# Optimization experiments

Measured on AMD Instinct MI355X. Metric: run time of the kernel, lower is better.

The kernel has to match this reference:

```python
import jax, jax.numpy as jnp
import numpy as np

B, S, Hd = 4, 2048, 1024
NH, D = 16, 64

def setup_inputs() -> dict:
    key = jax.random.key(0)
    ks = jax.random.split(key, 8)
    scale = 0.02
    return {
        "hidden_states": jax.random.normal(ks[0], (B, S, Hd), dtype=jnp.float32),
        "attention_mask": jnp.zeros((B, 1, 1, S), dtype=jnp.float32),
        "relations": jax.random.normal(ks[1], (1, 1, S, D), dtype=jnp.float32),
        "Wq": jax.random.normal(ks[2], (Hd, Hd), dtype=jnp.float32) * scale,
        "bq": jnp.zeros((Hd,), dtype=jnp.float32),
        "Wk": jax.random.normal(ks[3], (Hd, Hd), dtype=jnp.float32) * scale,
        "bk": jnp.zeros((Hd,), dtype=jnp.float32),
        "Wv": jax.random.normal(ks[4], (Hd, Hd), dtype=jnp.float32) * scale,
        "bv": jnp.zeros((Hd,), dtype=jnp.float32),
    }

def _heads(x):  # [B,S,Hd] -> [B,NH,S,D]
    return x.reshape(x.shape[0], x.shape[1], NH, D).transpose(0, 2, 1, 3)

def _rotate_half_interleaved(x):
    # stack([-x_odd, x_even], -1).reshape_as(x)
    return jnp.stack([-x[..., 1::2], x[..., ::2]], axis=-1).reshape(x.shape)

def reference(hidden_states, attention_mask, relations, Wq, bq, Wk, bk, Wv, bv):
    q = _heads(hidden_states @ Wq.T + bq)
    k = _heads(hidden_states @ Wk.T + bk)
    v = _heads(hidden_states @ Wv.T + bv)

    # interleaved rotary: cos from odd slots, sin from even slots, each repeated x2
    cos_pos = jnp.repeat(relations[..., 1::2], 2, axis=-1)  # [1,1,S,D]
    sin_pos = jnp.repeat(relations[..., ::2], 2, axis=-1)
    q = q * cos_pos + _rotate_half_interleaved(q) * sin_pos
    k = k * cos_pos + _rotate_half_interleaved(k) * sin_pos

    scores = jnp.einsum("bhqd,bhkd->bhqk", q, k) / jnp.sqrt(jnp.float32(D))
    scores = scores + attention_mask
    probs = jax.nn.softmax(scores, axis=-1)
    ctx = jnp.einsum("bhqk,bhkd->bhqd", probs, v)
    return ctx.transpose(0, 2, 1, 3).reshape(hidden_states.shape[0], hidden_states.shape[1], NH * D)
```

## Files before the change

### kernel.cpp

```cpp
#include <hip/hip_runtime.h>

typedef __attribute__((ext_vector_type(8))) short short8;
typedef __attribute__((ext_vector_type(4))) float f32x4;
typedef __attribute__((ext_vector_type(4))) unsigned int u32x4;
typedef __attribute__((ext_vector_type(2))) unsigned int u32x2;
typedef __attribute__((ext_vector_type(4))) unsigned short u16x4;
typedef __attribute__((ext_vector_type(2))) float f32x2;

#define NHEADS 16
#define DHEAD 64
#define SEQ 2048
#define BATCH 4
#define HD 1024
#define MTOT 8192

static __device__ __forceinline__ unsigned short f2b(float x) {
  unsigned u = __builtin_bit_cast(unsigned, x);
  u += 0x7fffu + ((u >> 16) & 1u);
  return (unsigned short)(u >> 16);
}

static __device__ __forceinline__ unsigned pk2(float lo, float hi) {
  unsigned a = __builtin_bit_cast(unsigned, lo);
  unsigned b = __builtin_bit_cast(unsigned, hi);
  a += 0x7fffu + ((a >> 16) & 1u);
  b += 0x7fffu + ((b >> 16) & 1u);
  return (a >> 16) | (b & 0xffff0000u);
}

static __device__ __forceinline__ void gll16(const void* g, void* l) {
  __builtin_amdgcn_global_load_lds(
      (const __attribute__((address_space(1))) unsigned int*)g,
      (__attribute__((address_space(3))) unsigned int*)l, 16, 0, 0);
}

__global__ void cvt_bf16(const float* __restrict__ src,
                         unsigned short* __restrict__ dst, int n4) {
  int i = blockIdx.x * blockDim.x + threadIdx.x;
  if (i < n4) {
    f32x4 v = ((const f32x4*)src)[i];
    u16x4 o;
    o[0] = f2b(v[0]); o[1] = f2b(v[1]); o[2] = f2b(v[2]); o[3] = f2b(v[3]);
    ((u16x4*)dst)[i] = o;
  }
}

__global__ __launch_bounds__(256) void qkv_gemm(
    const unsigned short* __restrict__ X,
    const unsigned short* __restrict__ Wall,
    const float* __restrict__ bq, const float* __restrict__ bk,
    const float* __restrict__ bv,
    const float* __restrict__ rel,
    unsigned short* __restrict__ Qo,
    unsigned short* __restrict__ Ko,
    unsigned short* __restrict__ Vt) {
  __shared__ __align__(16) unsigned short As[128 * 32];
  __shared__ __align__(16) unsigned short Bs[128 * 32];

  const int t = threadIdx.x;
  const int lane = t & 63;
  const int w = t >> 6;

  const int n = blockIdx.x;
  const int xcd = n & 7;
  const int li = n >> 3;
  const int pp = xcd * 3 + (li >> 6);
  const int bx = li & 63;
  const int by = pp & 7;
  const int bz = pp >> 3;

  const unsigned short* W = Wall + (size_t)bz * HD * HD;
  const int m0 = bx * 128;
  const int n0 = by * 128;

  f32x4 acc[4][4];
  for (int i = 0; i < 4; i++)
    for (int j = 0; j < 4; j++) acc[i][j] = (f32x4){0.f, 0.f, 0.f, 0.f};

  const int wm = (w & 1) * 64;
  const int wn = (w >> 1) * 64;
  const int cl = lane & 15;
  const int qd = lane >> 4;

  const int srow = lane >> 2;
  const int scol = (lane & 3) * 8;

  for (int k0 = 0; k0 < HD; k0 += 32) {
    __syncthreads();
#pragma unroll
    for (int j = 0; j < 2; j++) {
      int r0 = j * 64 + w * 16;
      gll16(X + (size_t)(m0 + r0 + srow) * HD + k0 + scol, As + r0 * 32);
      gll16(W + (size_t)(n0 + r0 + srow) * HD + k0 + scol, Bs + r0 * 32);
    }
    __syncthreads();

    const int fk = qd * 8;
    short8 af[4], bf[4];
#pragma unroll
    for (int i = 0; i < 4; i++)
      af[i] = *(const short8*)(As + (wm + i * 16 + cl) * 32 + fk);
#pragma unroll
    for (int j = 0; j < 4; j++)
      bf[j] = *(const short8*)(Bs + (wn + j * 16 + cl) * 32 + fk);
#pragma unroll
    for (int i = 0; i < 4; i++)
#pragma unroll
      for (int j = 0; j < 4; j++)
        acc[i][j] = __builtin_amdgcn_mfma_f32_16x16x32_bf16(af[i], bf[j],
                                                            acc[i][j], 0, 0, 0);
  }

  if (bz == 2) {
#pragma unroll
    for (int i = 0; i < 4; i++) {
#pragma unroll
      for (int j = 0; j < 4; j++) {
        int nn = n0 + wn + j * 16 + cl;
        int hh = nn >> 6, dd = nn & 63;
        int m = m0 + wm + i * 16 + qd * 4;
        int bb = m >> 11, ss = m & (SEQ - 1);
        float bn = bv[nn];
        u16x4 pk;
#pragma unroll
        for (int r = 0; r < 4; r++) pk[r] = f2b(acc[i][j][r] + bn);
        *(u16x4*)(Vt + ((size_t)((bb * NHEADS + hh) * DHEAD + dd)) * SEQ + ss) = pk;
      }
    }
  } else {
    const float* bias = (bz == 0) ? bq : bk;
    unsigned short* Out = (bz == 0) ? Qo : Ko;
#pragma unroll
    for (int i = 0; i < 4; i++) {
#pragma unroll
      for (int j = 0; j < 4; j++) {
        int nn = n0 + wn + j * 16 + cl;
        int hh = nn >> 6, dd = nn & 63;
        float bn = bias[nn];
#pragma unroll
        for (int r = 0; r < 4; r++) {
          int m = m0 + wm + i * 16 + qd * 4 + r;
          int bb = m >> 11, ss = m & (SEQ - 1);
          float x = acc[i][j][r] + bn;
          float p = __shfl_xor(x, 1);
          f32x2 sc = *(const f32x2*)(rel + ss * DHEAD + (dd & ~1));
          float y = (dd & 1) ? (x * sc[1] + p * sc[0])
                             : (x * sc[1] - p * sc[0]);
          Out[(((size_t)(bb * NHEADS + hh)) * SEQ + ss) * DHEAD + dd] = f2b(y);
        }
      }
    }
  }
}

__global__ __launch_bounds__(256, 2) void attn(
    const unsigned short* __restrict__ Q,
    const unsigned short* __restrict__ K,
    const unsigned short* __restrict__ Vt,
    const float* __restrict__ mask,
    float* __restrict__ out) {
  __shared__ __align__(16) unsigned short Ks[2][128 * 64];
  __shared__ __align__(16) unsigned short Vs[2][64 * 128];

  const int t = threadIdx.x;
  const int lane = t & 63;
  const int w = t >> 6;

  const int n = blockIdx.x;
  const int xcd = n & 7;
  const int li = n >> 3;
  const int bh = xcd * 8 + (li >> 4);
  const int qt = li & 15;

  const int b = bh >> 4, h = bh & 15;
  const int s0 = qt * 128;
  const unsigned short* Qp = Q + (size_t)bh * SEQ * DHEAD;
  const unsigned short* Kp = K + (size_t)bh * SEQ * DHEAD;
  const unsigned short* Vp = Vt + (size_t)bh * DHEAD * SEQ;

  const int cl = lane & 15;
  const int qd = lane >> 4;

  short8 qf[2][2];
#pragma unroll
  for (int mt = 0; mt < 2; mt++)
#pragma unroll
    for (int ks = 0; ks < 2; ks++)
      qf[mt][ks] = *(const short8*)(Qp + (size_t)(s0 + w * 32 + mt * 16 + cl) * DHEAD +
                                    ks * 32 + qd * 8);

  short8 onef;
#pragma unroll
  for (int j = 0; j < 8; j++) onef[j] = (short)0x3F80;

  f32x4 ov[2][4];
  f32x4 ovl[2];
#pragma unroll
  for (int mt = 0; mt < 2; mt++) {
    ovl[mt] = (f32x4){0.f, 0.f, 0.f, 0.f};
#pragma unroll
    for (int dt = 0; dt < 4; dt++) ov[mt][dt] = (f32x4){0.f, 0.f, 0.f, 0.f};
  }

  const float SCL = 0.125f * 1.4426950408889634f;
  const float MLG = 1.4426950408889634f;

  auto stage = [&](int bi, int kt) {
#pragma unroll
    for (int j = 0; j < 4; j++) {
      int r0 = w * 32 + j * 8;
      int r = r0 + (lane >> 3);
      int c = (lane & 7) ^ (r & 7);
      gll16(Kp + (size_t)(kt + r) * DHEAD + c * 8, &Ks[bi][r0 * 64]);
    }
#pragma unroll
    for (int j = 0; j < 4; j++) {
      int r0 = w * 16 + j * 4;
      int r = r0 + (lane >> 4);
      int c = (lane & 15) ^ (r & 7);
      gll16(Vp + (size_t)r * SEQ + kt + c * 8, &Vs[bi][r0 * 128]);
    }
  };

  stage(0, 0);

  for (int it = 0; it < SEQ / 128; it++) {
    const int kt = it * 128;
    const int bi = it & 1;
    __syncthreads();
    if (it + 1 < SEQ / 128) stage(1 - bi, kt + 128);
    const unsigned short* Ksb = &Ks[bi][0];
    const unsigned short* Vsb = &Vs[bi][0];

    f32x4 sc[2][8];
#pragma unroll
    for (int mt = 0; mt < 2; mt++)
#pragma unroll
      for (int nt = 0; nt < 8; nt++) sc[mt][nt] = (f32x4){0.f, 0.f, 0.f, 0.f};
#pragma unroll
    for (int ks = 0; ks < 2; ks++) {
#pragma unroll
      for (int nt = 0; nt < 8; nt++) {
        int krow = nt * 16 + cl;
        short8 kf = *(const short8*)(Ksb + krow * 64 +
                                     (((ks * 4 + qd) ^ (krow & 7)) << 3));
        sc[0][nt] = __builtin_amdgcn_mfma_f32_16x16x32_bf16(kf, qf[0][ks], sc[0][nt], 0, 0, 0);
        sc[1][nt] = __builtin_amdgcn_mfma_f32_16x16x32_bf16(kf, qf[1][ks], sc[1][nt], 0, 0, 0);
      }
    }

    f32x4 mkv[8];
#pragma unroll
    for (int nt = 0; nt < 8; nt++) {
      f32x4 mk = *(const f32x4*)(mask + b * SEQ + kt + nt * 16 + qd * 4);
      mkv[nt][0] = mk[0] * MLG; mkv[nt][1] = mk[1] * MLG;
      mkv[nt][2] = mk[2] * MLG; mkv[nt][3] = mk[3] * MLG;
    }
    unsigned pw[2][8][2];
#pragma unroll
    for (int mt = 0; mt < 2; mt++) {
#pragma unroll
      for (int nt = 0; nt < 8; nt++) {
        float p0 = __builtin_amdgcn_exp2f(sc[mt][nt][0] * SCL + mkv[nt][0]);
        float p1 = __builtin_amdgcn_exp2f(sc[mt][nt][1] * SCL + mkv[nt][1]);
        float p2 = __builtin_amdgcn_exp2f(sc[mt][nt][2] * SCL + mkv[nt][2]);
        float p3 = __builtin_amdgcn_exp2f(sc[mt][nt][3] * SCL + mkv[nt][3]);
        pw[mt][nt][0] = pk2(p0, p1);
        pw[mt][nt][1] = pk2(p2, p3);
      }
    }

#pragma unroll
    for (int c = 0; c < 4; c++) {
      u32x4 bb0 = {pw[0][2 * c][0], pw[0][2 * c][1], pw[0][2 * c + 1][0], pw[0][2 * c + 1][1]};
      u32x4 bb1 = {pw[1][2 * c][0], pw[1][2 * c][1], pw[1][2 * c + 1][0], pw[1][2 * c + 1][1]};
      short8 bf0 = __builtin_bit_cast(short8, bb0);
      short8 bf1 = __builtin_bit_cast(short8, bb1);
      ovl[0] = __builtin_amdgcn_mfma_f32_16x16x32_bf16(onef, bf0, ovl[0], 0, 0, 0);
      ovl[1] = __builtin_amdgcn_mfma_f32_16x16x32_bf16(onef, bf1, ovl[1], 0, 0, 0);
#pragma unroll
      for (int dt = 0; dt < 4; dt++) {
        int vrow = dt * 16 + cl;
        int sw = vrow & 7;
        const unsigned short* vb = Vsb + vrow * 128 + ((qd & 1) << 2);
        u32x2 v0 = *(const u32x2*)(vb + (((4 * c + (qd >> 1)) ^ sw) << 3));
        u32x2 v1 = *(const u32x2*)(vb + (((4 * c + 2 + (qd >> 1)) ^ sw) << 3));
        u32x4 vv = {v0[0], v0[1], v1[0], v1[1]};
        short8 vf = __builtin_bit_cast(short8, vv);
        ov[0][dt] = __builtin_amdgcn_mfma_f32_16x16x32_bf16(vf, bf0, ov[0][dt], 0, 0, 0);
        ov[1][dt] = __builtin_amdgcn_mfma_f32_16x16x32_bf16(vf, bf1, ov[1][dt], 0, 0, 0);
      }
    }
  }

#pragma unroll
  for (int mt = 0; mt < 2; mt++) {
    float rl = 1.0f / ovl[mt][0];
    int s = s0 + w * 32 + mt * 16 + cl;
    float* ob = out + ((size_t)b * SEQ + s) * HD + h * DHEAD;
#pragma unroll
    for (int dt = 0; dt < 4; dt++) {
      f32x4 o;
      o[0] = ov[mt][dt][0] * rl;
      o[1] = ov[mt][dt][1] * rl;
      o[2] = ov[mt][dt][2] * rl;
      o[3] = ov[mt][dt][3] * rl;
      *(f32x4*)(ob + dt * 16 + qd * 4) = o;
    }
  }
}

extern "C" void kernel_launch(void* const* d_in, const int* in_sizes, int n_in,
                              void* d_out, int out_size, void* d_ws, size_t ws_size,
                              hipStream_t stream) {
  const float* hidden = (const float*)d_in[0];
  const float* mask   = (const float*)d_in[1];
  const float* rel    = (const float*)d_in[2];
  const float* Wq     = (const float*)d_in[3];
  const float* bq     = (const float*)d_in[4];
  const float* Wk     = (const float*)d_in[5];
  const float* bk     = (const float*)d_in[6];
  const float* Wv     = (const float*)d_in[7];
  const float* bv     = (const float*)d_in[8];
  float* out = (float*)d_out;

  unsigned short* Xb = (unsigned short*)d_ws;
  unsigned short* Wb = Xb + (size_t)MTOT * HD;
  unsigned short* Qb = Wb + (size_t)3 * HD * HD;
  unsigned short* Kb = Qb + (size_t)MTOT * HD;
  unsigned short* Vb = Kb + (size_t)MTOT * HD;

  {
    int n4 = MTOT * HD / 4;
    cvt_bf16<<<n4 / 256, 256, 0, stream>>>(hidden, Xb, n4);
  }
  {
    int n4 = HD * HD / 4;
    cvt_bf16<<<n4 / 256, 256, 0, stream>>>(Wq, Wb, n4);
    cvt_bf16<<<n4 / 256, 256, 0, stream>>>(Wk, Wb + (size_t)HD * HD, n4);
    cvt_bf16<<<n4 / 256, 256, 0, stream>>>(Wv, Wb + (size_t)2 * HD * HD, n4);
  }
  qkv_gemm<<<dim3(1536), 256, 0, stream>>>(Xb, Wb, bq, bk, bv, rel, Qb, Kb, Vb);
  attn<<<dim3(1024), 256, 0, stream>>>(Qb, Kb, Vb, mask, out);
}
```

Before: 310.0 us.

## Fold softmax scale and mask into QKV epilogue, simplify attention inner loop

The 1/sqrt(D)*log2e factor moves into Q and exp(mask) into V, so the attention loop computes exp2 of raw scores with no per-element scale or mask add. The row sum is taken with an MFMA against a bf16 exp(mask) vector. The Q/K GEMM swaps MFMA operands so the epilogue can do vectorised rotary and packed stores. V is stored in a permuted column order so each V fragment is one 16-byte LDS read. The rounding-to-nearest-even bf16 pack becomes a cheaper round-half-up, and there is no max subtraction, so very negative masks or large scores may lose precision.

```diff
diff --git a/kernel.cpp b/kernel.cpp
--- a/kernel.cpp
+++ b/kernel.cpp
@@ -5,7 +5,6 @@
 typedef __attribute__((ext_vector_type(4))) unsigned int u32x4;
 typedef __attribute__((ext_vector_type(2))) unsigned int u32x2;
 typedef __attribute__((ext_vector_type(4))) unsigned short u16x4;
-typedef __attribute__((ext_vector_type(2))) float f32x2;
 
 #define NHEADS 16
 #define DHEAD 64
@@ -20,11 +19,9 @@
   return (unsigned short)(u >> 16);
 }
 
-static __device__ __forceinline__ unsigned pk2(float lo, float hi) {
-  unsigned a = __builtin_bit_cast(unsigned, lo);
-  unsigned b = __builtin_bit_cast(unsigned, hi);
-  a += 0x7fffu + ((a >> 16) & 1u);
-  b += 0x7fffu + ((b >> 16) & 1u);
+static __device__ __forceinline__ unsigned pk2h(float lo, float hi) {
+  unsigned a = __builtin_bit_cast(unsigned, lo) + 0x8000u;
+  unsigned b = __builtin_bit_cast(unsigned, hi) + 0x8000u;
   return (a >> 16) | (b & 0xffff0000u);
 }
 
@@ -45,12 +42,19 @@
   }
 }
 
+__global__ void prep_wmask(const float* __restrict__ m,
+                           unsigned short* __restrict__ wm, int n) {
+  int i = blockIdx.x * blockDim.x + threadIdx.x;
+  if (i < n) wm[i] = f2b(__expf(m[i]));
+}
+
 __global__ __launch_bounds__(256) void qkv_gemm(
     const unsigned short* __restrict__ X,
     const unsigned short* __restrict__ Wall,
     const float* __restrict__ bq, const float* __restrict__ bk,
     const float* __restrict__ bv,
     const float* __restrict__ rel,
+    const float* __restrict__ mask,
     unsigned short* __restrict__ Qo,
     unsigned short* __restrict__ Ko,
     unsigned short* __restrict__ Vt) {
@@ -103,51 +107,72 @@
 #pragma unroll
     for (int j = 0; j < 4; j++)
       bf[j] = *(const short8*)(Bs + (wn + j * 16 + cl) * 32 + fk);
-#pragma unroll
-    for (int i = 0; i < 4; i++)
-#pragma unroll
-      for (int j = 0; j < 4; j++)
-        acc[i][j] = __builtin_amdgcn_mfma_f32_16x16x32_bf16(af[i], bf[j],
-                                                            acc[i][j], 0, 0, 0);
+    if (bz < 2) {
+#pragma unroll
+      for (int i = 0; i < 4; i++)
+#pragma unroll
+        for (int j = 0; j < 4; j++)
+          acc[i][j] = __builtin_amdgcn_mfma_f32_16x16x32_bf16(bf[j], af[i],
+                                                              acc[i][j], 0, 0, 0);
+    } else {
+#pragma unroll
+      for (int i = 0; i < 4; i++)
+#pragma unroll
+        for (int j = 0; j < 4; j++)
+          acc[i][j] = __builtin_amdgcn_mfma_f32_16x16x32_bf16(af[i], bf[j],
+                                                              acc[i][j], 0, 0, 0);
+    }
   }
 
   if (bz == 2) {
+    const int hh = (n0 + wn) >> 6;
 #pragma unroll
     for (int i = 0; i < 4; i++) {
+      int mb = m0 + wm + i * 16 + qd * 4;
+      int bb = mb >> 11, ssb = mb & (SEQ - 1);
+      f32x4 mk = *(const f32x4*)(mask + bb * SEQ + ssb);
+      f32x4 w4;
+#pragma unroll
+      for (int r = 0; r < 4; r++) w4[r] = __expf(mk[r]);
+      int colp = (ssb & ~31) | ((ssb & 12) << 1) | (((ssb >> 4) & 1) << 2);
 #pragma unroll
       for (int j = 0; j < 4; j++) {
         int nn = n0 + wn + j * 16 + cl;
-        int hh = nn >> 6, dd = nn & 63;
-        int m = m0 + wm + i * 16 + qd * 4;
-        int bb = m >> 11, ss = m & (SEQ - 1);
+        int dd = j * 16 + cl;
         float bn = bv[nn];
-        u16x4 pk;
-#pragma unroll
-        for (int r = 0; r < 4; r++) pk[r] = f2b(acc[i][j][r] + bn);
-        *(u16x4*)(Vt + ((size_t)((bb * NHEADS + hh) * DHEAD + dd)) * SEQ + ss) = pk;
+        u32x2 pk;
+        pk[0] = pk2h((acc[i][j][0] + bn) * w4[0], (acc[i][j][1] + bn) * w4[1]);
+        pk[1] = pk2h((acc[i][j][2] + bn) * w4[2], (acc[i][j][3] + bn) * w4[3]);
+        *(u32x2*)(Vt + ((size_t)((bb * NHEADS + hh) * DHEAD + dd)) * SEQ + colp) = pk;
       }
     }
   } else {
     const float* bias = (bz == 0) ? bq : bk;
     unsigned short* Out = (bz == 0) ? Qo : Ko;
-#pragma unroll
-    for (int i = 0; i < 4; i++) {
-#pragma unroll
-      for (int j = 0; j < 4; j++) {
-        int nn = n0 + wn + j * 16 + cl;
-        int hh = nn >> 6, dd = nn & 63;
-        float bn = bias[nn];
-#pragma unroll
-        for (int r = 0; r < 4; r++) {
-          int m = m0 + wm + i * 16 + qd * 4 + r;
-          int bb = m >> 11, ss = m & (SEQ - 1);
-          float x = acc[i][j][r] + bn;
-          float p = __shfl_xor(x, 1);
-          f32x2 sc = *(const f32x2*)(rel + ss * DHEAD + (dd & ~1));
-          float y = (dd & 1) ? (x * sc[1] + p * sc[0])
-                             : (x * sc[1] - p * sc[0]);
-          Out[(((size_t)(bb * NHEADS + hh)) * SEQ + ss) * DHEAD + dd] = f2b(y);
-        }
+    const float qs = (bz == 0) ? 0.125f * 1.4426950408889634f : 1.0f;
+    const int hh = (n0 + wn) >> 6;
+#pragma unroll
+    for (int j = 0; j < 4; j++) {
+      int nb = n0 + wn + j * 16 + qd * 4;
+      f32x4 b4 = *(const f32x4*)(bias + nb);
+      int ddb = j * 16 + qd * 4;
+#pragma unroll
+      for (int i = 0; i < 4; i++) {
+        int s = m0 + wm + i * 16 + cl;
+        int bb = s >> 11, ss = s & (SEQ - 1);
+        f32x4 rl = *(const f32x4*)(rel + ss * DHEAD + ddb);
+        float x0 = acc[i][j][0] + b4[0];
+        float x1 = acc[i][j][1] + b4[1];
+        float x2 = acc[i][j][2] + b4[2];
+        float x3 = acc[i][j][3] + b4[3];
+        float y0 = (x0 * rl[1] - x1 * rl[0]) * qs;
+        float y1 = (x1 * rl[1] + x0 * rl[0]) * qs;
+        float y2 = (x2 * rl[3] - x3 * rl[2]) * qs;
+        float y3 = (x3 * rl[3] + x2 * rl[2]) * qs;
+        u32x2 pk;
+        pk[0] = pk2h(y0, y1);
+        pk[1] = pk2h(y2, y3);
+        *(u32x2*)(Out + (((size_t)(bb * NHEADS + hh)) * SEQ + ss) * DHEAD + ddb) = pk;
       }
     }
   }
@@ -157,7 +182,7 @@
     const unsigned short* __restrict__ Q,
     const unsigned short* __restrict__ K,
     const unsigned short* __restrict__ Vt,
-    const float* __restrict__ mask,
+    const unsigned short* __restrict__ wmask,
     float* __restrict__ out) {
   __shared__ __align__(16) unsigned short Ks[2][128 * 64];
   __shared__ __align__(16) unsigned short Vs[2][64 * 128];
@@ -177,6 +202,7 @@
   const unsigned short* Qp = Q + (size_t)bh * SEQ * DHEAD;
   const unsigned short* Kp = K + (size_t)bh * SEQ * DHEAD;
   const unsigned short* Vp = Vt + (size_t)bh * DHEAD * SEQ;
+  const unsigned short* wmp = wmask + b * SEQ;
 
   const int cl = lane & 15;
   const int qd = lane >> 4;
@@ -189,10 +215,6 @@
       qf[mt][ks] = *(const short8*)(Qp + (size_t)(s0 + w * 32 + mt * 16 + cl) * DHEAD +
                                     ks * 32 + qd * 8);
 
-  short8 onef;
-#pragma unroll
-  for (int j = 0; j < 8; j++) onef[j] = (short)0x3F80;
-
   f32x4 ov[2][4];
   f32x4 ovl[2];
 #pragma unroll
@@ -201,9 +223,6 @@
 #pragma unroll
     for (int dt = 0; dt < 4; dt++) ov[mt][dt] = (f32x4){0.f, 0.f, 0.f, 0.f};
   }
-
-  const float SCL = 0.125f * 1.4426950408889634f;
-  const float MLG = 1.4426950408889634f;
 
   auto stage = [&](int bi, int kt) {
 #pragma unroll
@@ -232,6 +251,15 @@
     const unsigned short* Ksb = &Ks[bi][0];
     const unsigned short* Vsb = &Vs[bi][0];
 
+    short8 wf[4];
+#pragma unroll
+    for (int c = 0; c < 4; c++) {
+      u32x2 w0 = *(const u32x2*)(wmp + kt + c * 32 + qd * 4);
+      u32x2 w1 = *(const u32x2*)(wmp + kt + c * 32 + 16 + qd * 4);
+      u32x4 ww = {w0[0], w0[1], w1[0], w1[1]};
+      wf[c] = __builtin_bit_cast(short8, ww);
+    }
+
     f32x4 sc[2][8];
 #pragma unroll
     for (int mt = 0; mt < 2; mt++)
@@ -249,24 +277,17 @@
       }
     }
 
-    f32x4 mkv[8];
-#pragma unroll
-    for (int nt = 0; nt < 8; nt++) {
-      f32x4 mk = *(const f32x4*)(mask + b * SEQ + kt + nt * 16 + qd * 4);
-      mkv[nt][0] = mk[0] * MLG; mkv[nt][1] = mk[1] * MLG;
-      mkv[nt][2] = mk[2] * MLG; mkv[nt][3] = mk[3] * MLG;
-    }
     unsigned pw[2][8][2];
 #pragma unroll
     for (int mt = 0; mt < 2; mt++) {
 #pragma unroll
       for (int nt = 0; nt < 8; nt++) {
-        float p0 = __builtin_amdgcn_exp2f(sc[mt][nt][0] * SCL + mkv[nt][0]);
-        float p1 = __builtin_amdgcn_exp2f(sc[mt][nt][1] * SCL + mkv[nt][1]);
-        float p2 = __builtin_amdgcn_exp2f(sc[mt][nt][2] * SCL + mkv[nt][2]);
-        float p3 = __builtin_amdgcn_exp2f(sc[mt][nt][3] * SCL + mkv[nt][3]);
-        pw[mt][nt][0] = pk2(p0, p1);
-        pw[mt][nt][1] = pk2(p2, p3);
+        float p0 = __builtin_amdgcn_exp2f(sc[mt][nt][0]);
+        float p1 = __builtin_amdgcn_exp2f(sc[mt][nt][1]);
+        float p2 = __builtin_amdgcn_exp2f(sc[mt][nt][2]);
+        float p3 = __builtin_amdgcn_exp2f(sc[mt][nt][3]);
+        pw[mt][nt][0] = pk2h(p0, p1);
+        pw[mt][nt][1] = pk2h(p2, p3);
       }
     }
 
@@ -276,17 +297,13 @@
       u32x4 bb1 = {pw[1][2 * c][0], pw[1][2 * c][1], pw[1][2 * c + 1][0], pw[1][2 * c + 1][1]};
       short8 bf0 = __builtin_bit_cast(short8, bb0);
       short8 bf1 = __builtin_bit_cast(short8, bb1);
-      ovl[0] = __builtin_amdgcn_mfma_f32_16x16x32_bf16(onef, bf0, ovl[0], 0, 0, 0);
-      ovl[1] = __builtin_amdgcn_mfma_f32_16x16x32_bf16(onef, bf1, ovl[1], 0, 0, 0);
+      ovl[0] = __builtin_amdgcn_mfma_f32_16x16x32_bf16(wf[c], bf0, ovl[0], 0, 0, 0);
+      ovl[1] = __builtin_amdgcn_mfma_f32_16x16x32_bf16(wf[c], bf1, ovl[1], 0, 0, 0);
 #pragma unroll
       for (int dt = 0; dt < 4; dt++) {
         int vrow = dt * 16 + cl;
-        int sw = vrow & 7;
-        const unsigned short* vb = Vsb + vrow * 128 + ((qd & 1) << 2);
-        u32x2 v0 = *(const u32x2*)(vb + (((4 * c + (qd >> 1)) ^ sw) << 3));
-        u32x2 v1 = *(const u32x2*)(vb + (((4 * c + 2 + (qd >> 1)) ^ sw) << 3));
-        u32x4 vv = {v0[0], v0[1], v1[0], v1[1]};
-        short8 vf = __builtin_bit_cast(short8, vv);
+        short8 vf = *(const short8*)(Vsb + vrow * 128 +
+                                     (((c * 4 + qd) ^ (vrow & 7)) << 3));
         ov[0][dt] = __builtin_amdgcn_mfma_f32_16x16x32_bf16(vf, bf0, ov[0][dt], 0, 0, 0);
         ov[1][dt] = __builtin_amdgcn_mfma_f32_16x16x32_bf16(vf, bf1, ov[1][dt], 0, 0, 0);
       }
@@ -329,6 +346,7 @@
   unsigned short* Qb = Wb + (size_t)3 * HD * HD;
   unsigned short* Kb = Qb + (size_t)MTOT * HD;
   unsigned short* Vb = Kb + (size_t)MTOT * HD;
+  unsigned short* Wm = Vb + (size_t)MTOT * HD;
 
   {
     int n4 = MTOT * HD / 4;
@@ -340,6 +358,7 @@
     cvt_bf16<<<n4 / 256, 256, 0, stream>>>(Wk, Wb + (size_t)HD * HD, n4);
     cvt_bf16<<<n4 / 256, 256, 0, stream>>>(Wv, Wb + (size_t)2 * HD * HD, n4);
   }
-  qkv_gemm<<<dim3(1536), 256, 0, stream>>>(Xb, Wb, bq, bk, bv, rel, Qb, Kb, Vb);
-  attn<<<dim3(1024), 256, 0, stream>>>(Qb, Kb, Vb, mask, out);
-}
+  prep_wmask<<<(BATCH * SEQ) / 256, 256, 0, stream>>>(mask, Wm, BATCH * SEQ);
+  qkv_gemm<<<dim3(1536), 256, 0, stream>>>(Xb, Wb, bq, bk, bv, rel, mask, Qb, Kb, Vb);
+  attn<<<dim3(1024), 256, 0, stream>>>(Qb, Kb, Vb, Wm, out);
+}
```

Measured after the change: 326.9 us. 1.05x slower.
